# Kernel optimization log

Measured on AMD Instinct MI355X. Metric: run time of the kernel, lower is better.

The kernel has to match this reference:

```python
import jax, jax.numpy as jnp
import numpy as np

N_NODES = 50000
D = 100          # hidden_size == out_size
STEP = 1
B, N, L = 512, 64, 64
STDV = 1.0 / np.sqrt(D)


def _uniform(key, shape):
    return jax.random.uniform(key, shape, jnp.float32, -STDV, STDV)


def setup_inputs() -> dict:
    key = jax.random.key(0)
    ks = jax.random.split(key, 16)
    inp = {
        'adj_in': jax.random.uniform(ks[0], (B, N, N), jnp.float32),
        'adj_out': jax.random.uniform(ks[1], (B, N, N), jnp.float32),
        'item': jax.random.randint(ks[2], (B, N), 0, N_NODES, jnp.int32),
        'alias': jax.random.randint(ks[3], (B, L), 0, N, jnp.int32),
        'mask': jnp.ones((B, L), jnp.float32),
        'tar': jax.random.randint(ks[4], (B,), 0, N_NODES - 1, jnp.int32) + 1,
        # learned parameters
        'embedding': _uniform(ks[5], (N_NODES, D)),
        'W_in': _uniform(ks[6], (D, D)),
        'b_in': _uniform(ks[7], (D,)),
        'W_out': _uniform(ks[8], (D, D)),
        'b_out': _uniform(ks[9], (D,)),
        'gate_kernel': _uniform(ks[10], (3 * D, 2 * D)),
        'gate_bias': jnp.ones((2 * D,), jnp.float32),
        'cand_kernel': _uniform(ks[11], (3 * D, D)),
        'cand_bias': jnp.zeros((D,), jnp.float32),
        'nasr_w1': _uniform(ks[12], (D, D)),
        'nasr_w2': _uniform(ks[13], (D, D)),
        'nasr_v': _uniform(ks[14], (1, D)),
        'nasr_b': jnp.zeros((D,), jnp.float32),
    }
    return inp


def _ggnn(embedding, item, adj_in, adj_out, W_in, b_in, W_out, b_out,
          gate_kernel, gate_bias, cand_kernel, cand_bias):
    fin = embedding[item]                                 # [B, N, D]
    for _ in range(STEP):
        fi = jnp.einsum('bnd,de->bne', fin, W_in) + b_in   # [B, N, D]
        fo = jnp.einsum('bnd,de->bne', fin, W_out) + b_out
        av = jnp.concatenate([jnp.matmul(adj_in, fi), jnp.matmul(adj_out, fo)], axis=-1)  # [B, N, 2D]
        x = av.reshape(-1, 2 * D)
        h = fin.reshape(-1, D)
        # TF GRUCell math
        gates = jax.nn.sigmoid(jnp.concatenate([x, h], -1) @ gate_kernel + gate_bias)
        r, u = jnp.split(gates, 2, axis=-1)
        c = jnp.tanh(jnp.concatenate([x, r * h], -1) @ cand_kernel + cand_bias)
        fin = (u * h + (1.0 - u) * c).reshape(fin.shape)
    return fin


def _forward(adj_in, adj_out, mask, embedding, W_in, b_in, W_out, b_out,
             gate_kernel, gate_bias, cand_kernel, cand_bias,
             nasr_w1, nasr_w2, nasr_v, nasr_b, item, alias, tar):
    re = _ggnn(embedding, item, adj_in, adj_out, W_in, b_in, W_out, b_out,
               gate_kernel, gate_bias, cand_kernel, cand_bias)   # [B, N, D]
    bsz = re.shape[0]
    rm = jnp.sum(mask, axis=1).astype(jnp.int32)                 # [B]
    rows = jnp.arange(bsz)
    last_id = alias[rows, rm - 1]                                # [B]
    last_h = re[rows, last_id]                                   # [B, D]
    seq_h = jnp.take_along_axis(re, alias[..., None], axis=1)    # [B, L, D]
    last = last_h @ nasr_w1                                      # [B, D]
    seq = jnp.einsum('bld,de->ble', seq_h, nasr_w2)              # [B, L, D]
    m = jax.nn.sigmoid(last[:, None, :] + seq + nasr_b)          # [B, L, D]
    coef = (m @ nasr_v[0]) * mask                                # [B, L]
    ma = jnp.sum(coef[..., None] * seq_h, axis=1)                # [B, D]
    logits = ma @ embedding[1:].T                                # [B, n_nodes-1]
    labels = tar - 1
    logp = jax.nn.log_softmax(logits, axis=-1)
    loss = -jnp.mean(logp[rows, labels])
    return loss, logits


def reference(adj_in, adj_out, item, alias, mask, tar, embedding,
              W_in, b_in, W_out, b_out, gate_kernel, gate_bias,
              cand_kernel, cand_bias, nasr_w1, nasr_w2, nasr_v, nasr_b):
    return _forward(adj_in, adj_out, mask, embedding, W_in, b_in, W_out, b_out,
                    gate_kernel, gate_bias, cand_kernel, cand_bias,
                    nasr_w1, nasr_w2, nasr_v, nasr_b, item, alias, tar)
```

## Files before the change

kernel.cpp:

```cpp
#include <hip/hip_runtime.h>
#include <math.h>

#define BB    512
#define NNODE 64
#define LLEN  64
#define DD    100
#define NNODES 50000
#define NM1   49999
#define KP    128
#define KAV   224
#define KTOT  352
#define NCB   391
#define SHIFT 20.0f

typedef __attribute__((ext_vector_type(8))) short short8;
typedef __attribute__((ext_vector_type(4))) short short4_t;
typedef __attribute__((ext_vector_type(4))) float f32x4;
typedef unsigned short ushort_t;

__device__ __forceinline__ float sigm(float x) { return 1.0f / (1.0f + __expf(-x)); }
__device__ __forceinline__ float mytanh(float x) {
  x = fminf(15.0f, fmaxf(-15.0f, x));
  float e = __expf(-2.0f * x);
  return (1.0f - e) / (1.0f + e);
}
__device__ __forceinline__ float f4c(const float4& v, int k) { return ((const float*)&v)[k]; }
__device__ __forceinline__ ushort_t f2bf(float f) {
  union { float f; unsigned u; } v; v.f = f;
  unsigned r = v.u + 0x7FFF + ((v.u >> 16) & 1);
  return (ushort_t)(r >> 16);
}
__device__ __forceinline__ float bf2f(ushort_t s) {
  union { unsigned u; float f; } v; v.u = ((unsigned)s) << 16;
  return v.f;
}
__device__ __forceinline__ short8 cvt8(const float* __restrict__ p) {
  float4 v0 = *(const float4*)p, v1 = *(const float4*)(p + 4);
  short8 r;
  r[0] = (short)f2bf(v0.x); r[1] = (short)f2bf(v0.y);
  r[2] = (short)f2bf(v0.z); r[3] = (short)f2bf(v0.w);
  r[4] = (short)f2bf(v1.x); r[5] = (short)f2bf(v1.y);
  r[6] = (short)f2bf(v1.z); r[7] = (short)f2bf(v1.w);
  return r;
}

__global__ __launch_bounds__(256) void k_cvt_all(
    const float* __restrict__ emb,
    const float* __restrict__ Wi, const float* __restrict__ Wo,
    const float* __restrict__ gk, const float* __restrict__ ck,
    ushort_t* __restrict__ eb2, ushort_t* __restrict__ WioT,
    ushort_t* __restrict__ gkT, ushort_t* __restrict__ ckT,
    float* __restrict__ out)
{
  const int bid = blockIdx.x, t = threadIdx.x;
  if (bid == 0 && t == 0) out[0] = 0.0f;
  if (bid < 6250) {
    const int tid = bid * 256 + t;
    const int r = tid >> 5, c4 = (tid & 31) * 4;
    if (r >= NNODES) return;
    short4_t o = {0, 0, 0, 0};
    if (c4 < DD) {
      float4 v = *(const float4*)(emb + (size_t)r * DD + c4);
      o.x = (short)f2bf(f4c(v, 0)); o.y = (short)f2bf(f4c(v, 1));
      o.z = (short)f2bf(f4c(v, 2)); o.w = (short)f2bf(f4c(v, 3));
    }
    *(short4_t*)(eb2 + (size_t)r * KP + c4) = o;
    return;
  }
  const int rem = bid - 6250;
  const int y = rem / 287;
  const int idx = (rem - y * 287) * 256 + t;
  if (y == 0) {
    if (idx >= 208 * 128) return;
    int n = idx >> 7, k = idx & 127;
    float v = 0.0f;
    if (k < DD) {
      if (n < 100) v = Wi[k * DD + n];
      else if (n < 200) v = Wo[k * DD + (n - 100)];
    }
    WioT[idx] = f2bf(v);
  } else if (y == 1) {
    if (idx >= 208 * KTOT) return;
    int n = idx / KTOT, k = idx - n * KTOT;
    float v = 0.0f;
    if (n < 200) {
      if (k < KAV) { if (k < 200) v = gk[k * 200 + n]; }
      else { int kk = k - KAV; if (kk < 100) v = gk[(200 + kk) * 200 + n]; }
    }
    gkT[idx] = f2bf(v);
  } else {
    if (idx >= 112 * KTOT) return;
    int n = idx / KTOT, k = idx - n * KTOT;
    float v = 0.0f;
    if (n < 100) {
      if (k < KAV) { if (k < 200) v = ck[k * DD + n]; }
      else { int kk = k - KAV; if (kk < 100) v = ck[(200 + kk) * DD + n]; }
    }
    ckT[idx] = f2bf(v);
  }
}

__global__ __launch_bounds__(512) void k_fused(
    const ushort_t* __restrict__ eb2, const int* __restrict__ item,
    const ushort_t* __restrict__ WioT,
    const float* __restrict__ bi, const float* __restrict__ bo,
    const float* __restrict__ adj_in, const float* __restrict__ adj_out,
    const ushort_t* __restrict__ gkT, const float* __restrict__ gb,
    const ushort_t* __restrict__ ckT, const float* __restrict__ cbs,
    const int* __restrict__ alias_, const float* __restrict__ mask,
    const float* __restrict__ w1, const float* __restrict__ w2,
    const float* __restrict__ nv, const float* __restrict__ nb,
    ushort_t* __restrict__ mab)
{
  __shared__ __align__(16) char pool[106928];
  ushort_t (*s_f)[112][72] = (ushort_t (*)[112][72])(pool);
  ushort_t (*s_rh)[136]    = (ushort_t (*)[136])(pool);
  float    (*s_m)[104]     = (float (*)[104])(pool);
  ushort_t (*s_av)[232]    = (ushort_t (*)[232])(pool + 32256);
  float    (*s_fin)[104]   = (float (*)[104])(pool + 32256);
  ushort_t (*s_h)[136]     = (ushort_t (*)[136])(pool + 61952);
  float    (*s_u)[104]     = (float (*)[104])(pool + 79360);
  float* s_last   = (float*)(pool + 105984);
  float* s_coef   = (float*)(pool + 106400);
  int*   s_idx    = (int*)(pool + 106656);
  int*   s_lastid = (int*)(pool + 106912);

  const int t = threadIdx.x;
  const int w8 = t >> 6, lane = t & 63;
  const int rw = w8 & 3, ch = w8 >> 2;
  const int n16 = lane & 15, quad = lane >> 4;
  const int b = blockIdx.x;

  {
    const int row = t >> 3, seg = t & 7;
    const ushort_t* hsrc = eb2 + (size_t)item[b * 64 + row] * KP + seg * 16;
    *(short8*)&s_h[row][seg * 16]     = *(const short8*)(hsrc);
    *(short8*)&s_h[row][seg * 16 + 8] = *(const short8*)(hsrc + 8);
  }
  if (t >= 64 && t < 128) {
    const int r2 = t - 64;
#pragma unroll
    for (int c = 200; c < 224; ++c) s_av[r2][c] = 0;
  }
  for (int idx = t; idx < 2 * 12 * 64; idx += 512) {
    int which = idx / 768, rem = idx - which * 768;
    s_f[which][100 + rem / 64][rem & 63] = 0;
  }
  __syncthreads();

  short8 af[4];
#pragma unroll
  for (int ks = 0; ks < 4; ++ks)
    af[ks] = *(const short8*)&s_h[rw * 16 + n16][quad * 8 + ks * 32];

  {
    const int node0 = rw * 16 + quad * 4;
    const int s0 = ch ? 7 : 0, s1 = ch ? 13 : 7;
    for (int sub = s0; sub < s1; ++sub) {
      const ushort_t* brow = WioT + (size_t)(sub * 16 + n16) * KP + quad * 8;
      f32x4 acc = {0.0f, 0.0f, 0.0f, 0.0f};
#pragma unroll
      for (int ks = 0; ks < 4; ++ks)
        acc = __builtin_amdgcn_mfma_f32_16x16x32_bf16(af[ks], *(const short8*)(brow + ks * 32), acc, 0, 0, 0);
      const int col = sub * 16 + n16;
      if (col < 200) {
        const float bias = (col < 100) ? bi[col] : bo[col - 100];
        short4_t st;
#pragma unroll
        for (int r = 0; r < 4; ++r) ((ushort_t*)&st)[r] = f2bf(acc[r] + bias);
        const int which = (col < 100) ? 0 : 1;
        const int c = (col < 100) ? col : col - 100;
        *(short4_t*)&s_f[which][c][node0] = st;
      }
    }
  }
  __syncthreads();

  {
    const float* aX = (ch ? adj_out : adj_in)
                      + ((size_t)b * 64 + rw * 16 + n16) * 64 + quad * 8;
    short8 afX[2];
    afX[0] = cvt8(aX); afX[1] = cvt8(aX + 32);
    for (int sub = 0; sub < 7; ++sub) {
      const int col = sub * 16 + n16;
      const ushort_t* bX = &s_f[ch][col][quad * 8];
      f32x4 acc = {0.0f, 0.0f, 0.0f, 0.0f};
#pragma unroll
      for (int ks = 0; ks < 2; ++ks)
        acc = __builtin_amdgcn_mfma_f32_16x16x32_bf16(afX[ks], *(const short8*)(bX + ks * 32), acc, 0, 0, 0);
      if (col < 100) {
#pragma unroll
        for (int r = 0; r < 4; ++r)
          s_av[rw * 16 + quad * 4 + r][ch * 100 + col] = f2bf(acc[r]);
      }
    }
  }
  __syncthreads();

  if (t < 64) {
#pragma unroll
    for (int c = 100; c < 128; ++c) s_rh[t][c] = 0;
  }
  short8 afa[7];
#pragma unroll
  for (int ks = 0; ks < 7; ++ks)
    afa[ks] = *(const short8*)&s_av[rw * 16 + n16][quad * 8 + ks * 32];

  {
    const int s0 = ch ? 7 : 0, s1 = ch ? 13 : 7;
    for (int sub = s0; sub < s1; ++sub) {
      const ushort_t* brow = gkT + (size_t)(sub * 16 + n16) * KTOT + quad * 8;
      f32x4 acc = {0.0f, 0.0f, 0.0f, 0.0f};
#pragma unroll
      for (int ks = 0; ks < 7; ++ks)
        acc = __builtin_amdgcn_mfma_f32_16x16x32_bf16(afa[ks], *(const short8*)(brow + ks * 32), acc, 0, 0, 0);
#pragma unroll
      for (int ks = 0; ks < 4; ++ks)
        acc = __builtin_amdgcn_mfma_f32_16x16x32_bf16(af[ks], *(const short8*)(brow + KAV + ks * 32), acc, 0, 0, 0);
      const int col = sub * 16 + n16;
      if (col < 200) {
        const float bias = gb[col];
#pragma unroll
        for (int r = 0; r < 4; ++r) {
          const int row = rw * 16 + quad * 4 + r;
          const float g = sigm(acc[r] + bias);
          if (col < 100) s_rh[row][col] = f2bf(g * bf2f(s_h[row][col]));
          else           s_u[row][col - 100] = g;
        }
      }
    }
  }
  __syncthreads();

  short8 afr[4];
#pragma unroll
  for (int ks = 0; ks < 4; ++ks)
    afr[ks] = *(const short8*)&s_rh[rw * 16 + n16][quad * 8 + ks * 32];

  {
    const int s0 = ch ? 4 : 0, s1 = ch ? 7 : 4;
    for (int sub = s0; sub < s1; ++sub) {
      const ushort_t* brow = ckT + (size_t)(sub * 16 + n16) * KTOT + quad * 8;
      f32x4 acc = {0.0f, 0.0f, 0.0f, 0.0f};
#pragma unroll
      for (int ks = 0; ks < 7; ++ks)
        acc = __builtin_amdgcn_mfma_f32_16x16x32_bf16(afa[ks], *(const short8*)(brow + ks * 32), acc, 0, 0, 0);
#pragma unroll
      for (int ks = 0; ks < 4; ++ks)
        acc = __builtin_amdgcn_mfma_f32_16x16x32_bf16(afr[ks], *(const short8*)(brow + KAV + ks * 32), acc, 0, 0, 0);
      const int col = sub * 16 + n16;
      if (col < 100) {
        const float bias = cbs[col];
#pragma unroll
        for (int r = 0; r < 4; ++r) {
          const int row = rw * 16 + quad * 4 + r;
          const float c_ = mytanh(acc[r] + bias);
          const float u = s_u[row][col];
          const float hv = bf2f(s_h[row][col]);
          s_fin[row][col] = u * hv + (1.0f - u) * c_;
        }
      }
    }
  }
  __syncthreads();

  if (t < 64) {
    float v = mask[b * LLEN + t];
    v += __shfl_xor(v, 1, 64);  v += __shfl_xor(v, 2, 64);
    v += __shfl_xor(v, 4, 64);  v += __shfl_xor(v, 8, 64);
    v += __shfl_xor(v, 16, 64); v += __shfl_xor(v, 32, 64);
    if (t == 0) {
      int rm = (int)(v + 0.5f);
      *s_lastid = alias_[b * LLEN + rm - 1];
    }
  } else if (t < 128) {
    s_idx[t - 64] = alias_[b * LLEN + (t - 64)];
  }
  __syncthreads();

  if (t < DD) {
    const float* lh = s_fin[*s_lastid];
    float acc = 0.0f;
#pragma unroll 4
    for (int k = 0; k < DD; ++k) acc += lh[k] * w1[k * DD + t];
    s_last[t] = acc;
  }
  __syncthreads();

  {
    const int tx = t & 31, ty = t >> 5, cb4 = tx * 4;
    if (cb4 < DD) {
      float acc[4][4] = {};
      const float* frs[4] = { s_fin[s_idx[ty * 4 + 0]], s_fin[s_idx[ty * 4 + 1]],
                              s_fin[s_idx[ty * 4 + 2]], s_fin[s_idx[ty * 4 + 3]] };
      for (int k4 = 0; k4 < 25; ++k4) {
        float4 bv[4];
#pragma unroll
        for (int kk = 0; kk < 4; ++kk)
          bv[kk] = *(const float4*)(w2 + (size_t)(k4 * 4 + kk) * DD + cb4);
#pragma unroll
        for (int i = 0; i < 4; ++i) {
          float4 a = *(const float4*)(frs[i] + k4 * 4);
#pragma unroll
          for (int kk = 0; kk < 4; ++kk) {
            float av_ = f4c(a, kk);
#pragma unroll
            for (int j = 0; j < 4; ++j) acc[i][j] += av_ * f4c(bv[kk], j);
          }
        }
      }
#pragma unroll
      for (int i = 0; i < 4; ++i) {
        const int l = ty * 4 + i;
#pragma unroll
        for (int j = 0; j < 4; ++j) {
          const int e = cb4 + j;
          s_m[l][e] = sigm(acc[i][j] + s_last[e] + nb[e]);
        }
      }
    }
  }
  __syncthreads();

  if (t < LLEN) {
    float acc = 0.0f;
#pragma unroll 4
    for (int e = 0; e < DD; ++e) acc += s_m[t][e] * nv[e];
    s_coef[t] = acc * mask[b * LLEN + t];
  }
  __syncthreads();

  if (t < DD) {
    float acc = 0.0f;
#pragma unroll 4
    for (int l = 0; l < LLEN; ++l) acc += s_coef[l] * s_fin[s_idx[l]][t];
    mab[(size_t)b * KP + t] = f2bf(acc);
  } else if (t < KP) {
    mab[(size_t)b * KP + t] = 0;
  }
}

__global__ __launch_bounds__(256) void k_logits_mfma(
    const ushort_t* __restrict__ eb2, const ushort_t* __restrict__ mab,
    float* __restrict__ out, float* __restrict__ sump)
{
  __shared__ float s_o[16][512];
  const int t = threadIdx.x;
  const int wave = t >> 6, lane = t & 63;
  const int n16 = lane & 15, quad = lane >> 4;
  const int bid = blockIdx.x;
  const int xcd = bid & 7;
  const int j = bid >> 3;
  const int grpl = j >> 5;
  const int lgmax = (xcd < 2) ? 13 : 12;
  if (grpl >= lgmax) return;
  const int stripe = j & 31;
  const int cg = ((xcd < 2) ? xcd * 13 : 26 + (xcd - 2) * 12) + grpl;
  const int m0 = stripe * 16;
  const int cblk = cg * 4 + wave;

  short8 afr[4];
  const ushort_t* abase = mab + (size_t)(m0 + n16) * KP + quad * 8;
#pragma unroll
  for (int ks = 0; ks < 4; ++ks) afr[ks] = *(const short8*)(abase + ks * 32);

  float s[4] = {0.0f, 0.0f, 0.0f, 0.0f};
  if (cblk < NCB) {
#pragma unroll
    for (int sub = 0; sub < 8; ++sub) {
      const int c = cblk * 128 + sub * 16 + n16;
      const ushort_t* bbase = eb2 + (size_t)((c < NM1) ? (c + 1) : 0) * KP + quad * 8;
      f32x4 acc = {0.0f, 0.0f, 0.0f, 0.0f};
#pragma unroll
      for (int ks = 0; ks < 4; ++ks) {
        short8 bfr = *(const short8*)(bbase + ks * 32);
        acc = __builtin_amdgcn_mfma_f32_16x16x32_bf16(afr[ks], bfr, acc, 0, 0, 0);
      }
#pragma unroll
      for (int r = 0; r < 4; ++r) {
        s_o[quad * 4 + r][wave * 128 + sub * 16 + n16] = acc[r];
        if (c < NM1) s[r] += __expf(acc[r] - SHIFT);
      }
    }
  }
  __syncthreads();

  float* lgp = out + 1;
  const int half = t >> 7, tc = t & 127;
#pragma unroll
  for (int it = 0; it < 8; ++it) {
    const int row = it * 2 + half;
    const size_t gr = m0 + row;
    f32x4 v = *(const f32x4*)&s_o[row][tc * 4];
    const int c0 = cg * 512 + tc * 4;
    if (c0 + 3 < NM1) {
      __builtin_nontemporal_store(v, (f32x4*)(lgp + gr * NM1 + c0));
    } else {
#pragma unroll
      for (int e = 0; e < 4; ++e)
        if (c0 + e < NM1)
          __builtin_nontemporal_store(v[e], lgp + gr * NM1 + c0 + e);
    }
  }

  if (cblk < NCB) {
    const int row0 = m0 + quad * 4;
#pragma unroll
    for (int r = 0; r < 4; ++r) {
      float x = s[r];
      x += __shfl_xor(x, 1, 64);
      x += __shfl_xor(x, 2, 64);
      x += __shfl_xor(x, 4, 64);
      x += __shfl_xor(x, 8, 64);
      if (n16 == 0) sump[(size_t)(row0 + r) * NCB + cblk] = x;
    }
  }
}

__global__ __launch_bounds__(64) void k_lse_loss(
    const float* __restrict__ sump, float* __restrict__ out,
    const int* __restrict__ tar)
{
  const int r = blockIdx.x, t = threadIdx.x;
  float s = 0.0f;
  for (int i = t; i < NCB; i += 64) s += sump[(size_t)r * NCB + i];
  for (int m = 1; m < 64; m <<= 1) s += __shfl_xor(s, m, 64);
  if (t == 0) {
    int label = tar[r] - 1;
    const float* lg = out + 1;
    float rt = lg[(size_t)r * NM1 + label] - (logf(s) + SHIFT);
    atomicAdd(out, -rt / (float)BB);
  }
}

extern "C" void kernel_launch(void* const* d_in, const int* in_sizes, int n_in,
                              void* d_out, int out_size, void* d_ws, size_t ws_size,
                              hipStream_t stream)
{
  (void)in_sizes; (void)n_in; (void)out_size; (void)ws_size;
  const float* adj_in  = (const float*)d_in[0];
  const float* adj_out = (const float*)d_in[1];
  const int*   item    = (const int*)d_in[2];
  const int*   alias_  = (const int*)d_in[3];
  const float* mask    = (const float*)d_in[4];
  const int*   tar     = (const int*)d_in[5];
  const float* emb     = (const float*)d_in[6];
  const float* W_in    = (const float*)d_in[7];
  const float* b_in    = (const float*)d_in[8];
  const float* W_out   = (const float*)d_in[9];
  const float* b_out   = (const float*)d_in[10];
  const float* gk      = (const float*)d_in[11];
  const float* gb      = (const float*)d_in[12];
  const float* ck      = (const float*)d_in[13];
  const float* cbs     = (const float*)d_in[14];
  const float* w1      = (const float*)d_in[15];
  const float* w2      = (const float*)d_in[16];
  const float* nv      = (const float*)d_in[17];
  const float* nb      = (const float*)d_in[18];
  float* out = (float*)d_out;

  ushort_t* usw = (ushort_t*)d_ws;
  ushort_t* eb2  = usw;
  ushort_t* WioT = usw + 13740032;
  ushort_t* gkT  = usw + 13766656;
  ushort_t* ckT  = usw + 13839872;
  ushort_t* mab  = usw + 13879296;
  float* fpool   = (float*)(usw + 13944832);
  float* sump    = fpool + 3276800;

  k_cvt_all <<<dim3(7111), 256, 0, stream>>>(emb, W_in, W_out, gk, ck,
                                             eb2, WioT, gkT, ckT, out);
  k_fused   <<<dim3(512), 512, 0, stream>>>(eb2, item, WioT, b_in, b_out,
                                            adj_in, adj_out, gkT, gb, ckT, cbs,
                                            alias_, mask, w1, w2, nv, nb, mab);
  k_logits_mfma<<<dim3(3328), 256, 0, stream>>>(eb2, mab, out, sump);
  k_lse_loss<<<dim3(512), 64, 0, stream>>>(sump, out, tar);
}
```

Before: 326.8 us.

## Coarsen embedding conversion, shrink fused LDS, atomically reduce row sums, single-block loss

The embedding-to-bf16 conversion now has each thread handle a 32-column chunk instead of 4 columns, cutting the conversion grid from 6250 to 782 blocks. The fused kernel stores the update gate as bf16 instead of float, shrinking shared memory from about 107KB to 80KB, which may let more blocks share a CU. The logits kernel atomically accumulates per-row exp sums into a 512-entry array instead of writing 391 partials per row. The loss then runs as one 512-thread block with a deterministic in-block reduction instead of per-row atomics, at the cost of atomic contention in the logits kernel and slightly lower gate precision.

```diff
diff --git a/kernel.cpp b/kernel.cpp
--- a/kernel.cpp
+++ b/kernel.cpp
@@ -50,24 +50,32 @@
     const float* __restrict__ gk, const float* __restrict__ ck,
     ushort_t* __restrict__ eb2, ushort_t* __restrict__ WioT,
     ushort_t* __restrict__ gkT, ushort_t* __restrict__ ckT,
-    float* __restrict__ out)
+    float* __restrict__ sumrow)
 {
   const int bid = blockIdx.x, t = threadIdx.x;
-  if (bid == 0 && t == 0) out[0] = 0.0f;
-  if (bid < 6250) {
+  if (bid < 782) {
     const int tid = bid * 256 + t;
-    const int r = tid >> 5, c4 = (tid & 31) * 4;
+    const int r = tid >> 2;
     if (r >= NNODES) return;
-    short4_t o = {0, 0, 0, 0};
-    if (c4 < DD) {
-      float4 v = *(const float4*)(emb + (size_t)r * DD + c4);
-      o.x = (short)f2bf(f4c(v, 0)); o.y = (short)f2bf(f4c(v, 1));
-      o.z = (short)f2bf(f4c(v, 2)); o.w = (short)f2bf(f4c(v, 3));
-    }
-    *(short4_t*)(eb2 + (size_t)r * KP + c4) = o;
+    const int c0 = (tid & 3) * 32;
+#pragma unroll
+    for (int c4 = c0; c4 < c0 + 32; c4 += 4) {
+      short4_t o = {0, 0, 0, 0};
+      if (c4 < DD) {
+        float4 v = *(const float4*)(emb + (size_t)r * DD + c4);
+        o.x = (short)f2bf(f4c(v, 0)); o.y = (short)f2bf(f4c(v, 1));
+        o.z = (short)f2bf(f4c(v, 2)); o.w = (short)f2bf(f4c(v, 3));
+      }
+      *(short4_t*)(eb2 + (size_t)r * KP + c4) = o;
+    }
     return;
   }
-  const int rem = bid - 6250;
+  if (bid == 1643) {
+    sumrow[t] = 0.0f;
+    sumrow[t + 256] = 0.0f;
+    return;
+  }
+  const int rem = bid - 782;
   const int y = rem / 287;
   const int idx = (rem - y * 287) * 256 + t;
   if (y == 0) {
@@ -112,18 +120,18 @@
     const float* __restrict__ nv, const float* __restrict__ nb,
     ushort_t* __restrict__ mab)
 {
-  __shared__ __align__(16) char pool[106928];
+  __shared__ __align__(16) char pool[80320];
   ushort_t (*s_f)[112][72] = (ushort_t (*)[112][72])(pool);
   ushort_t (*s_rh)[136]    = (ushort_t (*)[136])(pool);
+  ushort_t (*s_ub)[104]    = (ushort_t (*)[104])(pool + 17408);
   float    (*s_m)[104]     = (float (*)[104])(pool);
   ushort_t (*s_av)[232]    = (ushort_t (*)[232])(pool + 32256);
   float    (*s_fin)[104]   = (float (*)[104])(pool + 32256);
   ushort_t (*s_h)[136]     = (ushort_t (*)[136])(pool + 61952);
-  float    (*s_u)[104]     = (float (*)[104])(pool + 79360);
-  float* s_last   = (float*)(pool + 105984);
-  float* s_coef   = (float*)(pool + 106400);
-  int*   s_idx    = (int*)(pool + 106656);
-  int*   s_lastid = (int*)(pool + 106912);
+  float* s_last   = (float*)(pool + 79360);
+  float* s_coef   = (float*)(pool + 79776);
+  int*   s_idx    = (int*)(pool + 80032);
+  int*   s_lastid = (int*)(pool + 80288);
 
   const int t = threadIdx.x;
   const int w8 = t >> 6, lane = t & 63;
@@ -225,7 +233,7 @@
           const int row = rw * 16 + quad * 4 + r;
           const float g = sigm(acc[r] + bias);
           if (col < 100) s_rh[row][col] = f2bf(g * bf2f(s_h[row][col]));
-          else           s_u[row][col - 100] = g;
+          else           s_ub[row][col - 100] = f2bf(g);
         }
       }
     }
@@ -255,7 +263,7 @@
         for (int r = 0; r < 4; ++r) {
           const int row = rw * 16 + quad * 4 + r;
           const float c_ = mytanh(acc[r] + bias);
-          const float u = s_u[row][col];
+          const float u = bf2f(s_ub[row][col]);
           const float hv = bf2f(s_h[row][col]);
           s_fin[row][col] = u * hv + (1.0f - u) * c_;
         }
@@ -342,7 +350,7 @@
 
 __global__ __launch_bounds__(256) void k_logits_mfma(
     const ushort_t* __restrict__ eb2, const ushort_t* __restrict__ mab,
-    float* __restrict__ out, float* __restrict__ sump)
+    float* __restrict__ out, float* __restrict__ sumrow)
 {
   __shared__ float s_o[16][512];
   const int t = threadIdx.x;
@@ -412,24 +420,28 @@
       x += __shfl_xor(x, 2, 64);
       x += __shfl_xor(x, 4, 64);
       x += __shfl_xor(x, 8, 64);
-      if (n16 == 0) sump[(size_t)(row0 + r) * NCB + cblk] = x;
-    }
-  }
-}
-
-__global__ __launch_bounds__(64) void k_lse_loss(
-    const float* __restrict__ sump, float* __restrict__ out,
+      if (n16 == 0) atomicAdd(&sumrow[row0 + r], x);
+    }
+  }
+}
+
+__global__ __launch_bounds__(512) void k_lse_loss(
+    const float* __restrict__ sumrow, float* __restrict__ out,
     const int* __restrict__ tar)
 {
-  const int r = blockIdx.x, t = threadIdx.x;
-  float s = 0.0f;
-  for (int i = t; i < NCB; i += 64) s += sump[(size_t)r * NCB + i];
-  for (int m = 1; m < 64; m <<= 1) s += __shfl_xor(s, m, 64);
-  if (t == 0) {
-    int label = tar[r] - 1;
-    const float* lg = out + 1;
-    float rt = lg[(size_t)r * NM1 + label] - (logf(s) + SHIFT);
-    atomicAdd(out, -rt / (float)BB);
+  const int r = threadIdx.x;
+  __shared__ float red[8];
+  const float* lg = out + 1;
+  const int label = tar[r] - 1;
+  float rt = lg[(size_t)r * NM1 + label] - (logf(sumrow[r]) + SHIFT);
+  for (int m = 1; m < 64; m <<= 1) rt += __shfl_xor(rt, m, 64);
+  if ((r & 63) == 0) red[r >> 6] = rt;
+  __syncthreads();
+  if (r == 0) {
+    float tot = 0.0f;
+#pragma unroll
+    for (int i = 0; i < 8; ++i) tot += red[i];
+    out[0] = -tot / (float)BB;
   }
 }
 
@@ -466,13 +478,13 @@
   ushort_t* ckT  = usw + 13839872;
   ushort_t* mab  = usw + 13879296;
   float* fpool   = (float*)(usw + 13944832);
-  float* sump    = fpool + 3276800;
-
-  k_cvt_all <<<dim3(7111), 256, 0, stream>>>(emb, W_in, W_out, gk, ck,
-                                             eb2, WioT, gkT, ckT, out);
+  float* sumrow  = fpool + 3276800;
+
+  k_cvt_all <<<dim3(1644), 256, 0, stream>>>(emb, W_in, W_out, gk, ck,
+                                             eb2, WioT, gkT, ckT, sumrow);
   k_fused   <<<dim3(512), 512, 0, stream>>>(eb2, item, WioT, b_in, b_out,
                                             adj_in, adj_out, gkT, gb, ckT, cbs,
                                             alias_, mask, w1, w2, nv, nb, mab);
-  k_logits_mfma<<<dim3(3328), 256, 0, stream>>>(eb2, mab, out, sump);
-  k_lse_loss<<<dim3(512), 64, 0, stream>>>(sump, out, tar);
-}
+  k_logits_mfma<<<dim3(3328), 256, 0, stream>>>(eb2, mab, out, sumrow);
+  k_lse_loss<<<dim3(1), 512, 0, stream>>>(sumrow, out, tar);
+}
```

Result: faster. 312.4 us (-4.4%).
